# Optimization experiments

Hardware: AMD Instinct MI355X
Metric: run time of the kernel (lower is better)

Reference implementation:

```python
import jax, jax.numpy as jnp
import numpy as np

BLOCK = 128

def _dequant(w, scale, block):
    # w: [E, O, I] quantized values; scale: [E, ceil(O/block), ceil(I/block)]
    E, O, I = w.shape
    s = jnp.repeat(jnp.repeat(scale, block, axis=1)[:, :O], block, axis=2)[:, :, :I]
    return w * s

def setup_inputs() -> dict:
    key = jax.random.key(0)
    ks = jax.random.split(key, 7)
    T, H, F, E, K = 2048, 2048, 1024, 8, 2
    hidden_states = jax.random.normal(ks[0], (T, H), dtype=jnp.float32)
    topk_weights = jax.random.uniform(ks[1], (T, K), dtype=jnp.float32)
    topk_weights = topk_weights / jnp.sum(topk_weights, axis=-1, keepdims=True)
    topk_ids = jax.random.randint(ks[2], (T, K), 0, E, dtype=jnp.int64)
    gate_up_weight = jax.random.normal(ks[3], (E, 2 * F, H), dtype=jnp.float32) * 0.02
    gate_up_scale = jax.random.uniform(ks[4], (E, (2 * F) // BLOCK, H // BLOCK), dtype=jnp.float32)
    down_weight = jax.random.normal(ks[5], (E, H, F), dtype=jnp.float32) * 0.02
    down_scale = jax.random.uniform(ks[6], (E, H // BLOCK, F // BLOCK), dtype=jnp.float32)
    return dict(hidden_states=hidden_states, topk_weights=topk_weights,
                topk_ids=topk_ids, gate_up_weight=gate_up_weight,
                gate_up_scale=gate_up_scale, down_weight=down_weight,
                down_scale=down_scale)

def reference(hidden_states, topk_weights, topk_ids, gate_up_weight,
              gate_up_scale, down_weight, down_scale):
    T, H = hidden_states.shape
    E = gate_up_weight.shape[0]
    F = down_weight.shape[2]
    # blocked-fp8 dequant (scale_inv expanded over 128x128 blocks)
    w_gu = _dequant(gate_up_weight, gate_up_scale, BLOCK)   # [E, 2F, H]
    w_dn = _dequant(down_weight, down_scale, BLOCK)          # [E, H, F]
    # grouped gemm, expressed dense over experts
    h = jnp.einsum('th,eoh->teo', hidden_states, w_gu)       # [T, E, 2F]
    gate, up = h[..., :F], h[..., F:]
    act = jax.nn.silu(gate) * up                             # [T, E, F]
    out_e = jnp.einsum('tef,ehf->teh', act, w_dn)            # [T, E, H]
    # combine weights: scatter topk_weights into per-expert slots
    cw = jnp.zeros((T, E), dtype=hidden_states.dtype)
    cw = cw.at[jnp.arange(T)[:, None], topk_ids].add(topk_weights)
    return jnp.einsum('te,teh->th', cw, out_e)               # [T, H]
```

## Files before the change

kernel.cpp:

```cpp
#include <hip/hip_runtime.h>
#include <hip/hip_bf16.h>

#define T_TOK 2048
#define HDIM  2048
#define FDIM  1024
#define NEXP  8
#define KSEL  2
#define NENT  (T_TOK*KSEL)
#define WMAX1 26
#define WMAX2 40
#define PREPB 8192

typedef __attribute__((ext_vector_type(8))) short   short8v;
typedef __attribute__((ext_vector_type(4))) float   floatx4;
typedef __attribute__((ext_vector_type(4))) unsigned short ushort4v;

__device__ __forceinline__ unsigned short f2bf(float f) {
  unsigned int u = __builtin_bit_cast(unsigned int, f);
  u += 0x7FFFu + ((u >> 16) & 1u);
  return (unsigned short)(u >> 16);
}

__device__ __forceinline__ short8v cvt8(floatx4 v0, floatx4 v1, float sc) {
  short8v r = { (short)f2bf(v0.x*sc), (short)f2bf(v0.y*sc),
                (short)f2bf(v0.z*sc), (short)f2bf(v0.w*sc),
                (short)f2bf(v1.x*sc), (short)f2bf(v1.y*sc),
                (short)f2bf(v1.z*sc), (short)f2bf(v1.w*sc) };
  return r;
}

__device__ __forceinline__ void gll16(const void* g, void* l) {
  __builtin_amdgcn_global_load_lds(
      (const __attribute__((address_space(1))) unsigned int*)g,
      (__attribute__((address_space(3))) unsigned int*)l, 16, 0, 0);
}

#define ETOK_OFF 128

__global__ __launch_bounds__(256) void k_zero(float* __restrict__ p) {
  const int N = T_TOK * HDIM / 4;
  for (int c = blockIdx.x * 256 + threadIdx.x; c < N; c += 2048 * 256) {
    floatx4 z = {0.f, 0.f, 0.f, 0.f};
    *(floatx4*)(p + (size_t)c * 4) = z;
  }
}

__global__ void k_route(const int* __restrict__ ids, const float* __restrict__ tw,
                        int* __restrict__ wsI) {
  __shared__ int cnt[8], off[8], cur[8];
  const int tid = threadIdx.x;
  if (tid < 8) { cnt[tid] = 0; cur[tid] = 0; }
  __syncthreads();
  for (int g = tid; g < NENT; g += 256)
    atomicAdd(&cnt[ids[g] & 7], 1);
  __syncthreads();
  if (tid == 0) {
    int s = 0, n1 = 0, n2 = 0;
    int* wl1 = wsI + 48;
    int* wl2 = wsI + 96;
    for (int e = 0; e < 8; e++) {
      off[e] = s; wsI[16 + e] = s; wsI[e] = cnt[e];
      int c = cnt[e]; s += c;
      int nb1 = (c + 127) >> 7;
      for (int rb = 0; rb < nb1; rb++) wl1[n1++] = (e << 8) | rb;
      int nb2 = (c + 255) >> 8;
      for (int rb = 0; rb < nb2; rb++) wl2[n2++] = (e << 8) | rb;
    }
    wsI[24] = n1; wsI[25] = n2;
  }
  __syncthreads();
  int*   etok = wsI + ETOK_OFF;
  float* ew   = (float*)(wsI + ETOK_OFF + NENT);
  int*   inv  = wsI + ETOK_OFF + 2 * NENT;
  for (int g = tid; g < NENT; g += 256) {
    int e = ids[g] & 7;
    int pos = atomicAdd(&cur[e], 1);
    int idx = off[e] + pos;
    etok[idx] = g >> 1;
    ew[idx]   = tw[g];
    inv[g]    = idx;
  }
}

__global__ __launch_bounds__(256) void k_prep(const float* __restrict__ h,
                                              unsigned short* __restrict__ hb,
                                              const float* __restrict__ w,
                                              const float* __restrict__ s,
                                              unsigned short* __restrict__ wgb,
                                              const int* __restrict__ ids,
                                              const float* __restrict__ tw,
                                              int* __restrict__ wsI) {
  if (blockIdx.x == PREPB) {
    __shared__ int cnt[8], off[8], cur[8];
    const int tid = threadIdx.x;
    if (tid < 8) { cnt[tid] = 0; cur[tid] = 0; }
    __syncthreads();
    for (int g = tid; g < NENT; g += 256)
      atomicAdd(&cnt[ids[g] & 7], 1);
    __syncthreads();
    if (tid == 0) {
      int sum = 0, n1 = 0, n2 = 0;
      int* wl1 = wsI + 48;
      int* wl2 = wsI + 96;
      for (int e = 0; e < 8; e++) {
        off[e] = sum; wsI[16 + e] = sum; wsI[e] = cnt[e];
        int c = cnt[e]; sum += c;
        int nb1 = (c + 127) >> 7;
        for (int rb = 0; rb < nb1; rb++) wl1[n1++] = (e << 8) | rb;
        int nb2 = (c + 255) >> 8;
        for (int rb = 0; rb < nb2; rb++) wl2[n2++] = (e << 8) | rb;
      }
      wsI[24] = n1; wsI[25] = n2;
    }
    __syncthreads();
    int*   etok = wsI + ETOK_OFF;
    float* ew   = (float*)(wsI + ETOK_OFF + NENT);
    int*   inv  = wsI + ETOK_OFF + 2 * NENT;
    for (int g = threadIdx.x; g < NENT; g += 256) {
      int e = ids[g] & 7;
      int pos = atomicAdd(&cur[e], 1);
      int idx = off[e] + pos;
      etok[idx] = g >> 1;
      ew[idx]   = tw[g];
      inv[g]    = idx;
    }
    return;
  }

  const int gid = blockIdx.x * 256 + threadIdx.x;
  const int NH = T_TOK * HDIM / 8;
  if (gid < NH) {
    const floatx4 v0 = *(const floatx4*)(h + (size_t)gid * 8);
    const floatx4 v1 = *(const floatx4*)(h + (size_t)gid * 8 + 4);
    *(short8v*)(hb + (size_t)gid * 8) = cvt8(v0, v1, 1.f);
  }
  const int NG = NEXP * 2 * FDIM * HDIM / 8;
  for (int c = gid; c < NG; c += PREPB * 256) {
    int h8  = c & 255;
    int row = c >> 8;
    int e   = row >> 11;
    int orow = row & 2047;
    float sc = s[e * 256 + (orow >> 7) * 16 + (h8 >> 4)];
    const floatx4 v0 = *(const floatx4*)(w + (size_t)c * 8);
    const floatx4 v1 = *(const floatx4*)(w + (size_t)c * 8 + 4);
    *(short8v*)(wgb + (size_t)c * 8) = cvt8(v0, v1, sc);
  }
}

__global__ __launch_bounds__(256, 4) void k_gemm1n(
    const unsigned short* __restrict__ hb,
    const unsigned short* __restrict__ wgb,
    const int* __restrict__ wsI,
    unsigned short* __restrict__ act,
    const float* __restrict__ wdn,
    const float* __restrict__ sdn,
    unsigned short* __restrict__ wdb)
{
  const int nW = wsI[25];
  if ((int)blockIdx.x >= nW) {
    const int nIdle = 32 * (WMAX1 - nW);
    const int wid   = (int)blockIdx.y * (WMAX1 - nW) + ((int)blockIdx.x - nW);
    const int N = NEXP * HDIM * FDIM / 8;
    for (int c = wid * 256 + threadIdx.x; c < N; c += nIdle * 256) {
      int f8  = c & 127;
      int row = c >> 7;
      int e   = row >> 11;
      int h   = row & 2047;
      float sc = sdn[e * 128 + (h >> 7) * 8 + (f8 >> 4)];
      const floatx4 v0 = __builtin_nontemporal_load((const floatx4*)(wdn + (size_t)c * 8));
      const floatx4 v1 = __builtin_nontemporal_load((const floatx4*)(wdn + (size_t)c * 8 + 4));
      __builtin_nontemporal_store(cvt8(v0, v1, sc), (short8v*)(wdb + (size_t)c * 8));
    }
    return;
  }

  const int item = wsI[96 + blockIdx.x];
  const int e    = item >> 8;
  const int r0   = (item & 255) << 8;
  const int cnt  = wsI[e];
  const int off  = wsI[16 + e];
  const int c0   = blockIdx.y * 32;
  const int* etok = wsI + ETOK_OFF;

  __shared__ unsigned short As[256][64];
  __shared__ unsigned short Bs[64][64];

  const int tid = threadIdx.x, lane = tid & 63, w = tid >> 6;
  const int kg = lane >> 4, l15 = lane & 15, lr = lane >> 3, lc = lane & 7;

  unsigned int aoff[8];
#pragma unroll
  for (int i = 0; i < 8; i++) {
    int ra  = w * 64 + i * 8 + lr;
    int swz = (lc ^ (ra & 7)) * 8;
    int ent = r0 + ra; if (ent >= cnt) ent = cnt - 1;
    aoff[i] = (unsigned)etok[off + ent] * 2048u + (unsigned)swz;
  }
  unsigned int boff[2];
#pragma unroll
  for (int i = 0; i < 2; i++) {
    int rb  = (w * 2 + i) * 8 + lr;
    int swz = (lc ^ (rb & 7)) * 8;
    int gr  = (rb < 32) ? (c0 + rb) : (1024 + c0 + rb - 32);
    boff[i] = ((unsigned)e * 2048u + (unsigned)gr) * 2048u + (unsigned)swz;
  }

  floatx4 acc[4][4] = {};

  for (int k0 = 0; k0 < HDIM; k0 += 64) {
#pragma unroll
    for (int i = 0; i < 8; i++)
      gll16(hb + aoff[i] + k0, (char*)As + (w * 8 + i) * 1024);
#pragma unroll
    for (int i = 0; i < 2; i++)
      gll16(wgb + boff[i] + k0, (char*)Bs + (w * 2 + i) * 1024);
    __syncthreads();

    const char* Ab = (const char*)As;
    const char* Bb = (const char*)Bs;
#pragma unroll
    for (int ks = 0; ks < 2; ks++) {
      short8v a[4], b[4];
#pragma unroll
      for (int m = 0; m < 4; m++) {
        int r = w * 64 + m * 16 + l15;
        a[m] = *(const short8v*)(Ab + r * 128 + (((ks * 4 + kg) ^ (r & 7)) << 4));
      }
#pragma unroll
      for (int n = 0; n < 4; n++) {
        int rb = n * 16 + l15;
        b[n] = *(const short8v*)(Bb + rb * 128 + (((ks * 4 + kg) ^ (rb & 7)) << 4));
      }
#pragma unroll
      for (int m = 0; m < 4; m++)
#pragma unroll
        for (int n = 0; n < 4; n++)
          acc[m][n] = __builtin_amdgcn_mfma_f32_16x16x32_bf16(a[m], b[n], acc[m][n], 0, 0, 0);
    }
    __syncthreads();
  }

#pragma unroll
  for (int m = 0; m < 4; m++) {
    int rbase = r0 + w * 64 + m * 16 + kg * 4;
#pragma unroll
    for (int reg = 0; reg < 4; reg++) {
      int rr = rbase + reg;
      if (rr < cnt) {
#pragma unroll
        for (int n = 0; n < 2; n++) {
          float g = acc[m][n][reg];
          float u = acc[m][n + 2][reg];
          float a = g / (1.f + __expf(-g)) * u;
          act[(size_t)(off + rr) * FDIM + c0 + n * 16 + l15] = f2bf(a);
        }
      }
    }
  }
}

__global__ __launch_bounds__(256, 5) void k_gemm2n(
    const unsigned short* __restrict__ wdb,
    const int* __restrict__ wsI,
    const unsigned short* __restrict__ act,
    float* __restrict__ oe)
{
  if ((int)blockIdx.x >= wsI[24]) return;
  const int item = wsI[48 + blockIdx.x];
  const int e    = item >> 8;
  const int r0   = (item & 255) << 7;
  const int cnt  = wsI[e];
  const int off  = wsI[16 + e];
  const int c0   = blockIdx.y * 64;
  const float* ew = (const float*)(wsI + ETOK_OFF + NENT);

  __shared__ unsigned short As[128][64];
  __shared__ unsigned short Bs[64][64];

  const int tid = threadIdx.x, lane = tid & 63, w = tid >> 6;
  const int kg = lane >> 4, l15 = lane & 15, lr = lane >> 3, lc = lane & 7;
  const int wr = (w >> 1) * 64, wc = w & 1;

  unsigned int aoff[4];
#pragma unroll
  for (int i = 0; i < 4; i++) {
    int ra  = (w * 4 + i) * 8 + lr;
    int swz = (lc ^ (ra & 7)) * 8;
    int ent = r0 + ra; if (ent >= cnt) ent = cnt - 1;
    aoff[i] = (unsigned)(off + ent) * 1024u + (unsigned)swz;
  }
  unsigned int boff[2];
#pragma unroll
  for (int i = 0; i < 2; i++) {
    int rb  = (w * 2 + i) * 8 + lr;
    int swz = (lc ^ (rb & 7)) * 8;
    boff[i] = ((unsigned)e * 2048u + (unsigned)(c0 + rb)) * 1024u + (unsigned)swz;
  }

  floatx4 acc[4][2] = {};

  for (int k0 = 0; k0 < FDIM; k0 += 64) {
#pragma unroll
    for (int i = 0; i < 4; i++)
      gll16(act + aoff[i] + k0, (char*)As + (w * 4 + i) * 1024);
#pragma unroll
    for (int i = 0; i < 2; i++)
      gll16(wdb + boff[i] + k0, (char*)Bs + (w * 2 + i) * 1024);
    __syncthreads();

    const char* Ab = (const char*)As;
    const char* Bb = (const char*)Bs;
#pragma unroll
    for (int ks = 0; ks < 2; ks++) {
      short8v a[4], b[2];
#pragma unroll
      for (int m = 0; m < 4; m++) {
        int r = wr + m * 16 + l15;
        a[m] = *(const short8v*)(Ab + r * 128 + (((ks * 4 + kg) ^ (r & 7)) << 4));
      }
#pragma unroll
      for (int n = 0; n < 2; n++) {
        int rb = wc * 32 + n * 16 + l15;
        b[n] = *(const short8v*)(Bb + rb * 128 + (((ks * 4 + kg) ^ (rb & 7)) << 4));
      }
#pragma unroll
      for (int m = 0; m < 4; m++)
#pragma unroll
        for (int n = 0; n < 2; n++)
          acc[m][n] = __builtin_amdgcn_mfma_f32_16x16x32_bf16(a[m], b[n], acc[m][n], 0, 0, 0);
    }
    __syncthreads();
  }

#pragma unroll
  for (int m = 0; m < 4; m++) {
    int rbase = r0 + wr + m * 16 + kg * 4;
#pragma unroll
    for (int reg = 0; reg < 4; reg++) {
      int rr = rbase + reg;
      if (rr < cnt) {
        float wgt = ew[off + rr];
#pragma unroll
        for (int n = 0; n < 2; n++)
          oe[(size_t)(off + rr) * HDIM + c0 + wc * 32 + n * 16 + l15] =
              wgt * acc[m][n][reg];
      }
    }
  }
}

__global__ __launch_bounds__(256) void k_reduce(const int* __restrict__ wsI,
                                                const float* __restrict__ oe,
                                                float* __restrict__ out) {
  int i4 = blockIdx.x * 256 + threadIdx.x;
  if (i4 >= T_TOK * HDIM / 4) return;
  int t  = i4 >> 9;
  int h4 = (i4 & 511) * 4;
  const int* inv = wsI + ETOK_OFF + 2 * NENT;
  int e0 = inv[2 * t], e1 = inv[2 * t + 1];
  floatx4 a = *(const floatx4*)&oe[(size_t)e0 * HDIM + h4];
  floatx4 b = *(const floatx4*)&oe[(size_t)e1 * HDIM + h4];
  floatx4 r = a + b;
  *(floatx4*)&out[(size_t)t * HDIM + h4] = r;
}

__global__ __launch_bounds__(256) void k_gemm1_fb(
    const float* __restrict__ hidden, const float* __restrict__ wgu,
    const float* __restrict__ sgu, const int* __restrict__ wsI,
    unsigned short* __restrict__ act)
{
  const int e = blockIdx.y; const int cnt = wsI[e];
  const int r0 = blockIdx.x * 128; if (r0 >= cnt) return;
  const int off = wsI[16 + e]; const int c0 = blockIdx.z * 64;
  const int* etok = wsI + ETOK_OFF;
  __shared__ unsigned short As[128][40]; __shared__ unsigned short Bs[128][40];
  const int tid = threadIdx.x, lane = tid & 63, wv = tid >> 6;
  const int wr = (wv >> 1) * 64, wc = wv & 1, kg = lane >> 4, l15 = lane & 15;
  floatx4 acc[4][4] = {};
  for (int k0 = 0; k0 < HDIM; k0 += 32) {
#pragma unroll
    for (int c = tid; c < 1024; c += 256) {
      int row = c >> 3, k4 = c & 7;
      int rg = r0 + row; if (rg >= cnt) rg = cnt - 1;
      int tok = etok[off + rg];
      const floatx4 v = *(const floatx4*)&hidden[(size_t)tok * HDIM + k0 + k4 * 4];
      ushort4v o = { f2bf(v.x), f2bf(v.y), f2bf(v.z), f2bf(v.w) };
      *(ushort4v*)&As[row][k4 * 4] = o;
    }
#pragma unroll
    for (int c = tid; c < 1024; c += 256) {
      int row = c >> 3, k4 = c & 7;
      int gr = (row < 64) ? (c0 + row) : (FDIM + c0 + row - 64);
      float s = sgu[e * 256 + (gr >> 7) * 16 + (k0 >> 7)];
      const floatx4 v = *(const floatx4*)&wgu[((size_t)e * 2048 + gr) * HDIM + k0 + k4 * 4];
      ushort4v o = { f2bf(v.x * s), f2bf(v.y * s), f2bf(v.z * s), f2bf(v.w * s) };
      *(ushort4v*)&Bs[row][k4 * 4] = o;
    }
    __syncthreads();
    short8v a[4], b[4];
#pragma unroll
    for (int m = 0; m < 4; m++) a[m] = *(const short8v*)&As[wr + m * 16 + l15][kg * 8];
#pragma unroll
    for (int n = 0; n < 4; n++) {
      int br = (n < 2) ? (wc * 32 + n * 16) : (64 + wc * 32 + (n - 2) * 16);
      b[n] = *(const short8v*)&Bs[br + l15][kg * 8];
    }
#pragma unroll
    for (int m = 0; m < 4; m++)
#pragma unroll
      for (int n = 0; n < 4; n++)
        acc[m][n] = __builtin_amdgcn_mfma_f32_16x16x32_bf16(a[m], b[n], acc[m][n], 0, 0, 0);
    __syncthreads();
  }
#pragma unroll
  for (int m = 0; m < 4; m++) {
    int rbase = r0 + wr + m * 16 + kg * 4;
#pragma unroll
    for (int reg = 0; reg < 4; reg++) {
      int rr = rbase + reg;
      if (rr < cnt) {
#pragma unroll
        for (int n = 0; n < 2; n++) {
          float g = acc[m][n][reg], u = acc[m][n + 2][reg];
          float a = g / (1.f + expf(-g)) * u;
          act[(size_t)(off + rr) * FDIM + c0 + wc * 32 + n * 16 + l15] = f2bf(a);
        }
      }
    }
  }
}

__global__ __launch_bounds__(256) void k_gemm2_fb(
    const float* __restrict__ wdn, const float* __restrict__ sdn,
    const int* __restrict__ wsI, const unsigned short* __restrict__ act,
    float* __restrict__ out)
{
  const int e = blockIdx.y; const int cnt = wsI[e];
  const int r0 = blockIdx.x * 128; if (r0 >= cnt) return;
  const int off = wsI[16 + e]; const int c0 = blockIdx.z * 128;
  const int* etok = wsI + ETOK_OFF;
  const float* ew = (const float*)(wsI + ETOK_OFF + NENT);
  __shared__ unsigned short As[128][40]; __shared__ unsigned short Bs[128][40];
  const int tid = threadIdx.x, lane = tid & 63, wv = tid >> 6;
  const int wr = (wv >> 1) * 64, wc = wv & 1, kg = lane >> 4, l15 = lane & 15;
  floatx4 acc[4][4] = {};
  for (int k0 = 0; k0 < FDIM; k0 += 32) {
#pragma unroll
    for (int c = tid; c < 512; c += 256) {
      int row = c >> 2, k8 = c & 3;
      int rg = r0 + row; if (rg >= cnt) rg = cnt - 1;
      short8v v = *(const short8v*)&act[(size_t)(off + rg) * FDIM + k0 + k8 * 8];
      *(short8v*)&As[row][k8 * 8] = v;
    }
#pragma unroll
    for (int c = tid; c < 1024; c += 256) {
      int row = c >> 3, k4 = c & 7;
      int gr = c0 + row;
      float s = sdn[e * 128 + (gr >> 7) * 8 + (k0 >> 7)];
      const floatx4 v = *(const floatx4*)&wdn[((size_t)e * HDIM + gr) * FDIM + k0 + k4 * 4];
      ushort4v o = { f2bf(v.x * s), f2bf(v.y * s), f2bf(v.z * s), f2bf(v.w * s) };
      *(ushort4v*)&Bs[row][k4 * 4] = o;
    }
    __syncthreads();
    short8v a[4], b[4];
#pragma unroll
    for (int m = 0; m < 4; m++) a[m] = *(const short8v*)&As[wr + m * 16 + l15][kg * 8];
#pragma unroll
    for (int n = 0; n < 4; n++) b[n] = *(const short8v*)&Bs[wc * 64 + n * 16 + l15][kg * 8];
#pragma unroll
    for (int m = 0; m < 4; m++)
#pragma unroll
      for (int n = 0; n < 4; n++)
        acc[m][n] = __builtin_amdgcn_mfma_f32_16x16x32_bf16(a[m], b[n], acc[m][n], 0, 0, 0);
    __syncthreads();
  }
#pragma unroll
  for (int m = 0; m < 4; m++) {
    int rbase = r0 + wr + m * 16 + kg * 4;
#pragma unroll
    for (int reg = 0; reg < 4; reg++) {
      int rr = rbase + reg;
      if (rr < cnt) {
        int tok = etok[off + rr];
        float ww = ew[off + rr];
#pragma unroll
        for (int n = 0; n < 4; n++)
          atomicAdd(&out[(size_t)tok * HDIM + c0 + wc * 64 + n * 16 + l15], ww * acc[m][n][reg]);
      }
    }
  }
}

extern "C" void kernel_launch(void* const* d_in, const int* in_sizes, int n_in,
                              void* d_out, int out_size, void* d_ws, size_t ws_size,
                              hipStream_t stream) {
  const float* hidden = (const float*)d_in[0];
  const float* tw     = (const float*)d_in[1];
  const int*   ids    = (const int*)d_in[2];
  const float* wgu    = (const float*)d_in[3];
  const float* sgu    = (const float*)d_in[4];
  const float* wdn    = (const float*)d_in[5];
  const float* sdn    = (const float*)d_in[6];
  float* out = (float*)d_out;
  int* wsI = (int*)d_ws;

  const size_t NEED = 65536ull + (144ull << 20);
  if (ws_size >= NEED) {
    unsigned short* hb  = (unsigned short*)((char*)d_ws + 65536);
    unsigned short* wgb = hb  + (size_t)T_TOK * HDIM;
    unsigned short* wdb = wgb + (size_t)NEXP * 2 * FDIM * HDIM;
    unsigned short* act = wdb + (size_t)NEXP * HDIM * FDIM;
    float*          oe  = (float*)(act + (size_t)NENT * FDIM);

    k_prep<<<PREPB + 1, 256, 0, stream>>>(hidden, hb, wgu, sgu, wgb, ids, tw, wsI);

    dim3 g1(WMAX1, 32);
    k_gemm1n<<<g1, 256, 0, stream>>>(hb, wgb, wsI, act, wdn, sdn, wdb);
    dim3 g2(WMAX2, 32);
    k_gemm2n<<<g2, 256, 0, stream>>>(wdb, wsI, act, oe);
    k_reduce<<<T_TOK * HDIM / 4 / 256, 256, 0, stream>>>(wsI, oe, out);
  } else {
    k_zero <<<2048, 256, 0, stream>>>(out);
    k_route<<<1, 256, 0, stream>>>(ids, tw, wsI);
    unsigned short* act = (unsigned short*)((char*)d_ws + 65536);
    dim3 g1(NENT / 128, NEXP, FDIM / 64);
    k_gemm1_fb<<<g1, 256, 0, stream>>>(hidden, wgu, sgu, wsI, act);
    dim3 g2(NENT / 128, NEXP, HDIM / 128);
    k_gemm2_fb<<<g2, 256, 0, stream>>>(wdn, sdn, wsI, act, out);
  }
}
```

Baseline: 185.3 us.

## Give each wave a private LDS tile with register prefetch, dropping block syncs

Both grouped GEMM kernels now run 128-thread blocks in which each wave owns its own 64x64 A and B LDS tiles. Each wave prefetches the next K-slice into registers while it computes on the current slice, replacing global_load_lds and the __syncthreads barriers. GEMM1 switches to 128-row work items via a different routing table, and GEMM2 widens its per-wave N tile to 64. The change aims to remove barrier stalls and overlap global loads with MFMA work, at the cost of more registers, no B-tile sharing across waves, and the assumption that the routing table at wsI[48] and wsI[24] holds 128-row items. The idle-block down-weight conversion also drops its nontemporal hints.

```diff
diff --git a/kernel.cpp b/kernel.cpp
--- a/kernel.cpp
+++ b/kernel.cpp
@@ -7,8 +7,7 @@
 #define NEXP  8
 #define KSEL  2
 #define NENT  (T_TOK*KSEL)
-#define WMAX1 26
-#define WMAX2 40
+#define GX1   44
 #define PREPB 8192
 
 typedef __attribute__((ext_vector_type(8))) short   short8v;
@@ -27,12 +26,6 @@
                 (short)f2bf(v1.x*sc), (short)f2bf(v1.y*sc),
                 (short)f2bf(v1.z*sc), (short)f2bf(v1.w*sc) };
   return r;
-}
-
-__device__ __forceinline__ void gll16(const void* g, void* l) {
-  __builtin_amdgcn_global_load_lds(
-      (const __attribute__((address_space(1))) unsigned int*)g,
-      (__attribute__((address_space(3))) unsigned int*)l, 16, 0, 0);
 }
 
 #define ETOK_OFF 128
@@ -147,7 +140,7 @@
   }
 }
 
-__global__ __launch_bounds__(256, 4) void k_gemm1n(
+__global__ __launch_bounds__(128, 2) void k_gemm1n(
     const unsigned short* __restrict__ hb,
     const unsigned short* __restrict__ wgb,
     const int* __restrict__ wsI,
@@ -156,80 +149,81 @@
     const float* __restrict__ sdn,
     unsigned short* __restrict__ wdb)
 {
-  const int nW = wsI[25];
+  const int nW = wsI[24];
   if ((int)blockIdx.x >= nW) {
-    const int nIdle = 32 * (WMAX1 - nW);
-    const int wid   = (int)blockIdx.y * (WMAX1 - nW) + ((int)blockIdx.x - nW);
+    const int nIdle = 32 * (GX1 - nW);
+    const int wid   = (int)blockIdx.y * (GX1 - nW) + ((int)blockIdx.x - nW);
     const int N = NEXP * HDIM * FDIM / 8;
-    for (int c = wid * 256 + threadIdx.x; c < N; c += nIdle * 256) {
+    for (int c = wid * 128 + threadIdx.x; c < N; c += nIdle * 128) {
       int f8  = c & 127;
       int row = c >> 7;
       int e   = row >> 11;
       int h   = row & 2047;
       float sc = sdn[e * 128 + (h >> 7) * 8 + (f8 >> 4)];
-      const floatx4 v0 = __builtin_nontemporal_load((const floatx4*)(wdn + (size_t)c * 8));
-      const floatx4 v1 = __builtin_nontemporal_load((const floatx4*)(wdn + (size_t)c * 8 + 4));
-      __builtin_nontemporal_store(cvt8(v0, v1, sc), (short8v*)(wdb + (size_t)c * 8));
+      const floatx4 v0 = *(const floatx4*)(wdn + (size_t)c * 8);
+      const floatx4 v1 = *(const floatx4*)(wdn + (size_t)c * 8 + 4);
+      *(short8v*)(wdb + (size_t)c * 8) = cvt8(v0, v1, sc);
     }
     return;
   }
 
-  const int item = wsI[96 + blockIdx.x];
+  const int item = wsI[48 + blockIdx.x];
   const int e    = item >> 8;
-  const int r0   = (item & 255) << 8;
+  const int r0   = (item & 255) << 7;
   const int cnt  = wsI[e];
   const int off  = wsI[16 + e];
   const int c0   = blockIdx.y * 32;
   const int* etok = wsI + ETOK_OFF;
 
-  __shared__ unsigned short As[256][64];
-  __shared__ unsigned short Bs[64][64];
+  __shared__ unsigned short As[2][64][64];
+  __shared__ unsigned short Bs[2][64][64];
 
   const int tid = threadIdx.x, lane = tid & 63, w = tid >> 6;
-  const int kg = lane >> 4, l15 = lane & 15, lr = lane >> 3, lc = lane & 7;
-
-  unsigned int aoff[8];
+  const int kg = lane >> 4, l15 = lane & 15;
+  const int lr8 = lane >> 3, lc = lane & 7;
+  char* Aw = (char*)As[w];
+  char* Bw = (char*)Bs[w];
+
+  const unsigned short* asrc[8];
+  const unsigned short* bsrc[8];
+  int wadr[8];
 #pragma unroll
   for (int i = 0; i < 8; i++) {
-    int ra  = w * 64 + i * 8 + lr;
-    int swz = (lc ^ (ra & 7)) * 8;
-    int ent = r0 + ra; if (ent >= cnt) ent = cnt - 1;
-    aoff[i] = (unsigned)etok[off + ent] * 2048u + (unsigned)swz;
-  }
-  unsigned int boff[2];
-#pragma unroll
-  for (int i = 0; i < 2; i++) {
-    int rb  = (w * 2 + i) * 8 + lr;
-    int swz = (lc ^ (rb & 7)) * 8;
-    int gr  = (rb < 32) ? (c0 + rb) : (1024 + c0 + rb - 32);
-    boff[i] = ((unsigned)e * 2048u + (unsigned)gr) * 2048u + (unsigned)swz;
+    int ra  = i * 8 + lr8;
+    int ent = r0 + w * 64 + ra; if (ent >= cnt) ent = cnt - 1;
+    asrc[i] = hb + (size_t)etok[off + ent] * HDIM + lc * 8;
+    int gr  = (ra < 32) ? (c0 + ra) : (1024 + c0 + ra - 32);
+    bsrc[i] = wgb + ((size_t)e * 2048 + gr) * HDIM + lc * 8;
+    wadr[i] = ra * 128 + ((lc ^ (ra & 7)) << 4);
   }
 
   floatx4 acc[4][4] = {};
-
-  for (int k0 = 0; k0 < HDIM; k0 += 64) {
-#pragma unroll
-    for (int i = 0; i < 8; i++)
-      gll16(hb + aoff[i] + k0, (char*)As + (w * 8 + i) * 1024);
-#pragma unroll
-    for (int i = 0; i < 2; i++)
-      gll16(wgb + boff[i] + k0, (char*)Bs + (w * 2 + i) * 1024);
-    __syncthreads();
-
-    const char* Ab = (const char*)As;
-    const char* Bb = (const char*)Bs;
+  short8v av[8], bv[8];
+
+#pragma unroll
+  for (int i = 0; i < 8; i++) { av[i] = *(const short8v*)(asrc[i]); bv[i] = *(const short8v*)(bsrc[i]); }
+#pragma unroll
+  for (int i = 0; i < 8; i++) { *(short8v*)(Aw + wadr[i]) = av[i]; *(short8v*)(Bw + wadr[i]) = bv[i]; }
+
+  for (int t = 0; t < 32; ++t) {
+    if (t + 1 < 32) {
+      const int kn = (t + 1) * 64;
+#pragma unroll
+      for (int i = 0; i < 8; i++) { av[i] = *(const short8v*)(asrc[i] + kn); bv[i] = *(const short8v*)(bsrc[i] + kn); }
+      __builtin_amdgcn_sched_barrier(0);
+    }
 #pragma unroll
     for (int ks = 0; ks < 2; ks++) {
       short8v a[4], b[4];
 #pragma unroll
       for (int m = 0; m < 4; m++) {
-        int r = w * 64 + m * 16 + l15;
-        a[m] = *(const short8v*)(Ab + r * 128 + (((ks * 4 + kg) ^ (r & 7)) << 4));
+        int r = m * 16 + l15;
+        a[m] = *(const short8v*)(Aw + r * 128 + (((ks * 4 + kg) ^ (r & 7)) << 4));
       }
 #pragma unroll
       for (int n = 0; n < 4; n++) {
         int rb = n * 16 + l15;
-        b[n] = *(const short8v*)(Bb + rb * 128 + (((ks * 4 + kg) ^ (rb & 7)) << 4));
+        b[n] = *(const short8v*)(Bw + rb * 128 + (((ks * 4 + kg) ^ (rb & 7)) << 4));
       }
 #pragma unroll
       for (int m = 0; m < 4; m++)
@@ -237,7 +231,10 @@
         for (int n = 0; n < 4; n++)
           acc[m][n] = __builtin_amdgcn_mfma_f32_16x16x32_bf16(a[m], b[n], acc[m][n], 0, 0, 0);
     }
-    __syncthreads();
+    if (t + 1 < 32) {
+#pragma unroll
+      for (int i = 0; i < 8; i++) { *(short8v*)(Aw + wadr[i]) = av[i]; *(short8v*)(Bw + wadr[i]) = bv[i]; }
+    }
   }
 
 #pragma unroll
@@ -259,7 +256,7 @@
   }
 }
 
-__global__ __launch_bounds__(256, 5) void k_gemm2n(
+__global__ __launch_bounds__(128, 2) void k_gemm2n(
     const unsigned short* __restrict__ wdb,
     const int* __restrict__ wsI,
     const unsigned short* __restrict__ act,
@@ -274,76 +271,78 @@
   const int c0   = blockIdx.y * 64;
   const float* ew = (const float*)(wsI + ETOK_OFF + NENT);
 
-  __shared__ unsigned short As[128][64];
-  __shared__ unsigned short Bs[64][64];
+  __shared__ unsigned short As[2][64][64];
+  __shared__ unsigned short Bs[2][64][64];
 
   const int tid = threadIdx.x, lane = tid & 63, w = tid >> 6;
-  const int kg = lane >> 4, l15 = lane & 15, lr = lane >> 3, lc = lane & 7;
-  const int wr = (w >> 1) * 64, wc = w & 1;
-
-  unsigned int aoff[4];
-#pragma unroll
-  for (int i = 0; i < 4; i++) {
-    int ra  = (w * 4 + i) * 8 + lr;
-    int swz = (lc ^ (ra & 7)) * 8;
-    int ent = r0 + ra; if (ent >= cnt) ent = cnt - 1;
-    aoff[i] = (unsigned)(off + ent) * 1024u + (unsigned)swz;
-  }
-  unsigned int boff[2];
-#pragma unroll
-  for (int i = 0; i < 2; i++) {
-    int rb  = (w * 2 + i) * 8 + lr;
-    int swz = (lc ^ (rb & 7)) * 8;
-    boff[i] = ((unsigned)e * 2048u + (unsigned)(c0 + rb)) * 1024u + (unsigned)swz;
-  }
-
-  floatx4 acc[4][2] = {};
-
-  for (int k0 = 0; k0 < FDIM; k0 += 64) {
-#pragma unroll
-    for (int i = 0; i < 4; i++)
-      gll16(act + aoff[i] + k0, (char*)As + (w * 4 + i) * 1024);
-#pragma unroll
-    for (int i = 0; i < 2; i++)
-      gll16(wdb + boff[i] + k0, (char*)Bs + (w * 2 + i) * 1024);
-    __syncthreads();
-
-    const char* Ab = (const char*)As;
-    const char* Bb = (const char*)Bs;
+  const int kg = lane >> 4, l15 = lane & 15;
+  const int lr8 = lane >> 3, lc = lane & 7;
+  char* Aw = (char*)As[w];
+  char* Bw = (char*)Bs[w];
+
+  const unsigned short* asrc[8];
+  const unsigned short* bsrc[8];
+  int wadr[8];
+#pragma unroll
+  for (int i = 0; i < 8; i++) {
+    int ra  = i * 8 + lr8;
+    int ent = r0 + w * 64 + ra; if (ent >= cnt) ent = cnt - 1;
+    asrc[i] = act + (size_t)(off + ent) * FDIM + lc * 8;
+    bsrc[i] = wdb + ((size_t)e * 2048 + (c0 + ra)) * FDIM + lc * 8;
+    wadr[i] = ra * 128 + ((lc ^ (ra & 7)) << 4);
+  }
+
+  floatx4 acc[4][4] = {};
+  short8v av[8], bv[8];
+
+#pragma unroll
+  for (int i = 0; i < 8; i++) { av[i] = *(const short8v*)(asrc[i]); bv[i] = *(const short8v*)(bsrc[i]); }
+#pragma unroll
+  for (int i = 0; i < 8; i++) { *(short8v*)(Aw + wadr[i]) = av[i]; *(short8v*)(Bw + wadr[i]) = bv[i]; }
+
+  for (int t = 0; t < 16; ++t) {
+    if (t + 1 < 16) {
+      const int kn = (t + 1) * 64;
+#pragma unroll
+      for (int i = 0; i < 8; i++) { av[i] = *(const short8v*)(asrc[i] + kn); bv[i] = *(const short8v*)(bsrc[i] + kn); }
+      __builtin_amdgcn_sched_barrier(0);
+    }
 #pragma unroll
     for (int ks = 0; ks < 2; ks++) {
-      short8v a[4], b[2];
+      short8v a[4], b[4];
 #pragma unroll
       for (int m = 0; m < 4; m++) {
-        int r = wr + m * 16 + l15;
-        a[m] = *(const short8v*)(Ab + r * 128 + (((ks * 4 + kg) ^ (r & 7)) << 4));
-      }
-#pragma unroll
-      for (int n = 0; n < 2; n++) {
-        int rb = wc * 32 + n * 16 + l15;
-        b[n] = *(const short8v*)(Bb + rb * 128 + (((ks * 4 + kg) ^ (rb & 7)) << 4));
+        int r = m * 16 + l15;
+        a[m] = *(const short8v*)(Aw + r * 128 + (((ks * 4 + kg) ^ (r & 7)) << 4));
+      }
+#pragma unroll
+      for (int n = 0; n < 4; n++) {
+        int rb = n * 16 + l15;
+        b[n] = *(const short8v*)(Bw + rb * 128 + (((ks * 4 + kg) ^ (rb & 7)) << 4));
       }
 #pragma unroll
       for (int m = 0; m < 4; m++)
 #pragma unroll
-        for (int n = 0; n < 2; n++)
+        for (int n = 0; n < 4; n++)
           acc[m][n] = __builtin_amdgcn_mfma_f32_16x16x32_bf16(a[m], b[n], acc[m][n], 0, 0, 0);
     }
-    __syncthreads();
+    if (t + 1 < 16) {
+#pragma unroll
+      for (int i = 0; i < 8; i++) { *(short8v*)(Aw + wadr[i]) = av[i]; *(short8v*)(Bw + wadr[i]) = bv[i]; }
+    }
   }
 
 #pragma unroll
   for (int m = 0; m < 4; m++) {
-    int rbase = r0 + wr + m * 16 + kg * 4;
+    int rbase = r0 + w * 64 + m * 16 + kg * 4;
 #pragma unroll
     for (int reg = 0; reg < 4; reg++) {
       int rr = rbase + reg;
       if (rr < cnt) {
         float wgt = ew[off + rr];
 #pragma unroll
-        for (int n = 0; n < 2; n++)
-          oe[(size_t)(off + rr) * HDIM + c0 + wc * 32 + n * 16 + l15] =
-              wgt * acc[m][n][reg];
+        for (int n = 0; n < 4; n++)
+          oe[(size_t)(off + rr) * HDIM + c0 + n * 16 + l15] = wgt * acc[m][n][reg];
       }
     }
   }
@@ -514,10 +513,10 @@
 
     k_prep<<<PREPB + 1, 256, 0, stream>>>(hidden, hb, wgu, sgu, wgb, ids, tw, wsI);
 
-    dim3 g1(WMAX1, 32);
-    k_gemm1n<<<g1, 256, 0, stream>>>(hb, wgb, wsI, act, wdn, sdn, wdb);
-    dim3 g2(WMAX2, 32);
-    k_gemm2n<<<g2, 256, 0, stream>>>(wdb, wsI, act, oe);
+    dim3 g1(GX1, 32);
+    k_gemm1n<<<g1, 128, 0, stream>>>(hb, wgb, wsI, act, wdn, sdn, wdb);
+    dim3 g2(GX1, 32);
+    k_gemm2n<<<g2, 128, 0, stream>>>(wdb, wsI, act, oe);
     k_reduce<<<T_TOK * HDIM / 4 / 256, 256, 0, stream>>>(wsI, oe, out);
   } else {
     k_zero <<<2048, 256, 0, stream>>>(out);
```

Measured after the change: 221.7 us. 19.6% more time.

## Move down-weight dequant into prep kernel and enlarge gemm2 row tiles to 256

Applied to the files above, without the earlier changes.

The down-projection weight fp32-to-bf16 dequant moves out of the idle blocks of the first grouped GEMM and into the prep kernel, beside the gate/up weight conversion. The second GEMM now uses 256-row work items, reusing gemm1's work list, with each warp covering all 64 output columns. That doubles A-tile reuse per B load and cuts the number of blocks. The trade-off is that prep grows and runs serially before gemm1, losing the overlap with gemm1, while gemm2 uses more registers and LDS at lower occupancy.

```diff
diff --git a/kernel.cpp b/kernel.cpp
--- a/kernel.cpp
+++ b/kernel.cpp
@@ -7,8 +7,7 @@
 #define NEXP  8
 #define KSEL  2
 #define NENT  (T_TOK*KSEL)
-#define WMAX1 26
-#define WMAX2 40
+#define WMAX1 24
 #define PREPB 8192
 
 typedef __attribute__((ext_vector_type(8))) short   short8v;
@@ -87,6 +86,9 @@
                                               const float* __restrict__ w,
                                               const float* __restrict__ s,
                                               unsigned short* __restrict__ wgb,
+                                              const float* __restrict__ wdn,
+                                              const float* __restrict__ sdn,
+                                              unsigned short* __restrict__ wdb,
                                               const int* __restrict__ ids,
                                               const float* __restrict__ tw,
                                               int* __restrict__ wsI) {
@@ -145,35 +147,26 @@
     const floatx4 v1 = *(const floatx4*)(w + (size_t)c * 8 + 4);
     *(short8v*)(wgb + (size_t)c * 8) = cvt8(v0, v1, sc);
   }
+  const int ND = NEXP * HDIM * FDIM / 8;
+  for (int c = gid; c < ND; c += PREPB * 256) {
+    int f8  = c & 127;
+    int row = c >> 7;
+    int e   = row >> 11;
+    int hh  = row & 2047;
+    float sc = sdn[e * 128 + (hh >> 7) * 8 + (f8 >> 4)];
+    const floatx4 v0 = *(const floatx4*)(wdn + (size_t)c * 8);
+    const floatx4 v1 = *(const floatx4*)(wdn + (size_t)c * 8 + 4);
+    *(short8v*)(wdb + (size_t)c * 8) = cvt8(v0, v1, sc);
+  }
 }
 
 __global__ __launch_bounds__(256, 4) void k_gemm1n(
     const unsigned short* __restrict__ hb,
     const unsigned short* __restrict__ wgb,
     const int* __restrict__ wsI,
-    unsigned short* __restrict__ act,
-    const float* __restrict__ wdn,
-    const float* __restrict__ sdn,
-    unsigned short* __restrict__ wdb)
+    unsigned short* __restrict__ act)
 {
-  const int nW = wsI[25];
-  if ((int)blockIdx.x >= nW) {
-    const int nIdle = 32 * (WMAX1 - nW);
-    const int wid   = (int)blockIdx.y * (WMAX1 - nW) + ((int)blockIdx.x - nW);
-    const int N = NEXP * HDIM * FDIM / 8;
-    for (int c = wid * 256 + threadIdx.x; c < N; c += nIdle * 256) {
-      int f8  = c & 127;
-      int row = c >> 7;
-      int e   = row >> 11;
-      int h   = row & 2047;
-      float sc = sdn[e * 128 + (h >> 7) * 8 + (f8 >> 4)];
-      const floatx4 v0 = __builtin_nontemporal_load((const floatx4*)(wdn + (size_t)c * 8));
-      const floatx4 v1 = __builtin_nontemporal_load((const floatx4*)(wdn + (size_t)c * 8 + 4));
-      __builtin_nontemporal_store(cvt8(v0, v1, sc), (short8v*)(wdb + (size_t)c * 8));
-    }
-    return;
-  }
-
+  if ((int)blockIdx.x >= wsI[25]) return;
   const int item = wsI[96 + blockIdx.x];
   const int e    = item >> 8;
   const int r0   = (item & 255) << 8;
@@ -259,32 +252,31 @@
   }
 }
 
-__global__ __launch_bounds__(256, 5) void k_gemm2n(
+__global__ __launch_bounds__(256, 4) void k_gemm2n(
     const unsigned short* __restrict__ wdb,
     const int* __restrict__ wsI,
     const unsigned short* __restrict__ act,
     float* __restrict__ oe)
 {
-  if ((int)blockIdx.x >= wsI[24]) return;
-  const int item = wsI[48 + blockIdx.x];
+  if ((int)blockIdx.x >= wsI[25]) return;
+  const int item = wsI[96 + blockIdx.x];
   const int e    = item >> 8;
-  const int r0   = (item & 255) << 7;
+  const int r0   = (item & 255) << 8;
   const int cnt  = wsI[e];
   const int off  = wsI[16 + e];
   const int c0   = blockIdx.y * 64;
   const float* ew = (const float*)(wsI + ETOK_OFF + NENT);
 
-  __shared__ unsigned short As[128][64];
+  __shared__ unsigned short As[256][64];
   __shared__ unsigned short Bs[64][64];
 
   const int tid = threadIdx.x, lane = tid & 63, w = tid >> 6;
   const int kg = lane >> 4, l15 = lane & 15, lr = lane >> 3, lc = lane & 7;
-  const int wr = (w >> 1) * 64, wc = w & 1;
-
-  unsigned int aoff[4];
-#pragma unroll
-  for (int i = 0; i < 4; i++) {
-    int ra  = (w * 4 + i) * 8 + lr;
+
+  unsigned int aoff[8];
+#pragma unroll
+  for (int i = 0; i < 8; i++) {
+    int ra  = w * 64 + i * 8 + lr;
     int swz = (lc ^ (ra & 7)) * 8;
     int ent = r0 + ra; if (ent >= cnt) ent = cnt - 1;
     aoff[i] = (unsigned)(off + ent) * 1024u + (unsigned)swz;
@@ -297,12 +289,12 @@
     boff[i] = ((unsigned)e * 2048u + (unsigned)(c0 + rb)) * 1024u + (unsigned)swz;
   }
 
-  floatx4 acc[4][2] = {};
+  floatx4 acc[4][4] = {};
 
   for (int k0 = 0; k0 < FDIM; k0 += 64) {
 #pragma unroll
-    for (int i = 0; i < 4; i++)
-      gll16(act + aoff[i] + k0, (char*)As + (w * 4 + i) * 1024);
+    for (int i = 0; i < 8; i++)
+      gll16(act + aoff[i] + k0, (char*)As + (w * 8 + i) * 1024);
 #pragma unroll
     for (int i = 0; i < 2; i++)
       gll16(wdb + boff[i] + k0, (char*)Bs + (w * 2 + i) * 1024);
@@ -312,21 +304,21 @@
     const char* Bb = (const char*)Bs;
 #pragma unroll
     for (int ks = 0; ks < 2; ks++) {
-      short8v a[4], b[2];
+      short8v a[4], b[4];
 #pragma unroll
       for (int m = 0; m < 4; m++) {
-        int r = wr + m * 16 + l15;
+        int r = w * 64 + m * 16 + l15;
         a[m] = *(const short8v*)(Ab + r * 128 + (((ks * 4 + kg) ^ (r & 7)) << 4));
       }
 #pragma unroll
-      for (int n = 0; n < 2; n++) {
-        int rb = wc * 32 + n * 16 + l15;
+      for (int n = 0; n < 4; n++) {
+        int rb = n * 16 + l15;
         b[n] = *(const short8v*)(Bb + rb * 128 + (((ks * 4 + kg) ^ (rb & 7)) << 4));
       }
 #pragma unroll
       for (int m = 0; m < 4; m++)
 #pragma unroll
-        for (int n = 0; n < 2; n++)
+        for (int n = 0; n < 4; n++)
           acc[m][n] = __builtin_amdgcn_mfma_f32_16x16x32_bf16(a[m], b[n], acc[m][n], 0, 0, 0);
     }
     __syncthreads();
@@ -334,16 +326,15 @@
 
 #pragma unroll
   for (int m = 0; m < 4; m++) {
-    int rbase = r0 + wr + m * 16 + kg * 4;
+    int rbase = r0 + w * 64 + m * 16 + kg * 4;
 #pragma unroll
     for (int reg = 0; reg < 4; reg++) {
       int rr = rbase + reg;
       if (rr < cnt) {
         float wgt = ew[off + rr];
 #pragma unroll
-        for (int n = 0; n < 2; n++)
-          oe[(size_t)(off + rr) * HDIM + c0 + wc * 32 + n * 16 + l15] =
-              wgt * acc[m][n][reg];
+        for (int n = 0; n < 4; n++)
+          oe[(size_t)(off + rr) * HDIM + c0 + n * 16 + l15] = wgt * acc[m][n][reg];
       }
     }
   }
@@ -512,11 +503,12 @@
     unsigned short* act = wdb + (size_t)NEXP * HDIM * FDIM;
     float*          oe  = (float*)(act + (size_t)NENT * FDIM);
 
-    k_prep<<<PREPB + 1, 256, 0, stream>>>(hidden, hb, wgu, sgu, wgb, ids, tw, wsI);
+    k_prep<<<PREPB + 1, 256, 0, stream>>>(hidden, hb, wgu, sgu, wgb,
+                                          wdn, sdn, wdb, ids, tw, wsI);
 
     dim3 g1(WMAX1, 32);
-    k_gemm1n<<<g1, 256, 0, stream>>>(hb, wgb, wsI, act, wdn, sdn, wdb);
-    dim3 g2(WMAX2, 32);
+    k_gemm1n<<<g1, 256, 0, stream>>>(hb, wgb, wsI, act);
+    dim3 g2(WMAX1, 32);
     k_gemm2n<<<g2, 256, 0, stream>>>(wdb, wsI, act, oe);
     k_reduce<<<T_TOK * HDIM / 4 / 256, 256, 0, stream>>>(wsI, oe, out);
   } else {
```

Result: faster. 162.7 us, median of 2 (-12.2%).
